# Kernel tuning notes

Measured on AMD Instinct MI355X. Metric: run time of the kernel, lower is better.

## Reference

```python
import jax, jax.numpy as jnp
import numpy as np

EPS = 1e-5
L = 8      # n_layers
H = 1024   # n_hidden
F_IN = 26  # input features
B = 65536  # batch


def layer_norm(x, gamma, beta):
    m = jnp.mean(x, axis=-1, keepdims=True)
    v = jnp.mean((x - m) ** 2, axis=-1, keepdims=True)
    return (x - m) * jax.lax.rsqrt(v + EPS) * gamma + beta


def setup_inputs() -> dict:
    key = jax.random.key(0)
    ks = jax.random.split(key, 12)
    s_in = 1.0 / np.sqrt(F_IN)
    s_h = 1.0 / np.sqrt(H)
    return {
        "x": jax.random.normal(ks[0], (B, F_IN), jnp.float32),
        "st_gamma": jnp.ones((F_IN,), jnp.float32),
        "st_beta": jnp.zeros((F_IN,), jnp.float32),
        "st_w": jax.random.uniform(ks[1], (H, F_IN), jnp.float32, -s_in, s_in),
        "st_b": jax.random.uniform(ks[2], (H,), jnp.float32, -s_in, s_in),
        "blk_gamma": jnp.ones((L, H), jnp.float32),
        "blk_beta": jnp.zeros((L, H), jnp.float32),
        "blk_w": jax.random.uniform(ks[3], (L, H, H), jnp.float32, -s_h, s_h),
        "blk_b": jax.random.uniform(ks[4], (L, H), jnp.float32, -s_h, s_h),
        "last_gamma": jnp.ones((H,), jnp.float32),
        "last_beta": jnp.zeros((H,), jnp.float32),
        "last_w": jax.random.uniform(ks[5], (1, H), jnp.float32, -s_h, s_h),
        "last_b": jax.random.uniform(ks[6], (1,), jnp.float32, -s_h, s_h),
    }


def reference(x, st_gamma, st_beta, st_w, st_b,
              blk_gamma, blk_beta, blk_w, blk_b,
              last_gamma, last_beta, last_w, last_b):
    # Stem: LN(26) -> Linear(26->H) -> ReLU (dropout = identity in eval)
    h = jax.nn.relu(layer_norm(x, st_gamma, st_beta) @ st_w.T + st_b)

    # n_layers blocks: LN -> Linear(H->H) -> ReLU, scanned over stacked params
    def body(h, params):
        g, b, w, bb = params
        h = jax.nn.relu(layer_norm(h, g, b) @ w.T + bb)
        return h, None

    h, _ = jax.lax.scan(body, h, (blk_gamma, blk_beta, blk_w, blk_b))

    # Head: LN -> Linear(H->1) -> sigmoid
    h = layer_norm(h, last_gamma, last_beta)
    out = jax.nn.sigmoid(h @ last_w.T + last_b)  # [B, 1]
    return out
```

## Files before the change

kernel.cpp:

```cpp
#include <hip/hip_runtime.h>
#include <hip/hip_bf16.h>
#include <stdint.h>


typedef __attribute__((ext_vector_type(8))) _Float16 f16x8;
typedef __attribute__((ext_vector_type(4))) float f32x4;

#define EPSLN 1e-5f
#define HDIM 1024

__device__ __forceinline__ void gload16(const void* g, void* l) {
  __builtin_amdgcn_global_load_lds(
      (const __attribute__((address_space(1))) unsigned int*)g,
      (__attribute__((address_space(3))) unsigned int*)l, 16, 0, 0);
}

__global__ __launch_bounds__(256) void zero_f32(float* __restrict__ p, int n) {
  int i = blockIdx.x * 256 + threadIdx.x;
  if (i < n) p[i] = 0.f;
}

__global__ __launch_bounds__(256) void fold_blk(
    const float* __restrict__ bg, const float* __restrict__ bb,
    const float* __restrict__ bw, const float* __restrict__ bbias,
    float* __restrict__ bfold, float* __restrict__ Sfold) {
  int lo = blockIdx.x;
  int layer = lo >> 10;
  const float* wrow = bw + (size_t)lo * HDIM;
  const float* g = bg + (size_t)layer * HDIM;
  const float* be = bb + (size_t)layer * HDIM;
  int t = threadIdx.x;
  float s = 0.f, acb = 0.f;
  for (int i = t; i < HDIM; i += 256) {
    float wv = wrow[i];
    _Float16 wp = (_Float16)(wv * g[i]);
    s += (float)wp;
    acb += be[i] * wv;
  }
#pragma unroll
  for (int off = 1; off < 64; off <<= 1) { s += __shfl_xor(s, off); acb += __shfl_xor(acb, off); }
  __shared__ float rs[4], rb[4];
  int l = t & 63, w = t >> 6;
  if (l == 0) { rs[w] = s; rb[w] = acb; }
  __syncthreads();
  if (t == 0) {
    Sfold[lo] = rs[0] + rs[1] + rs[2] + rs[3];
    bfold[lo] = bbias[lo] + rb[0] + rb[1] + rb[2] + rb[3];
  }
}

__global__ __launch_bounds__(256) void fold_pack(
    const float* __restrict__ bg, const float* __restrict__ bw,
    _Float16* __restrict__ Wfrag) {
  size_t tid = (size_t)blockIdx.x * 256 + threadIdx.x;
  int lay = (int)(tid >> 17);
  int oct = (int)(tid & 131071);
  int frag = oct >> 6, lane = oct & 63;
  int n16 = frag >> 5, kc = frag & 31;
  int o = n16 * 16 + (lane & 15);
  int ibase = kc * 32 + ((lane >> 4) << 3);
  const float* wrow = bw + ((size_t)lay << 20) + (size_t)o * HDIM + ibase;
  const float* g = bg + (size_t)lay * HDIM + ibase;
  f16x8 v;
#pragma unroll
  for (int j = 0; j < 8; ++j) v[j] = (_Float16)(wrow[j] * g[j]);
  *(f16x8*)(Wfrag + tid * 8) = v;
}

__global__ __launch_bounds__(256) void fold_head(
    const float* __restrict__ lg, const float* __restrict__ lb,
    const float* __restrict__ lw, const float* __restrict__ lbias,
    float* __restrict__ headW, float* __restrict__ headAux) {
  int t = threadIdx.x;
  float s = 0.f, acb = 0.f;
  for (int i = t; i < HDIM; i += 256) {
    float wp = lw[i] * lg[i];
    headW[i] = wp;
    s += wp;
    acb += lb[i] * lw[i];
  }
#pragma unroll
  for (int off = 1; off < 64; off <<= 1) { s += __shfl_xor(s, off); acb += __shfl_xor(acb, off); }
  __shared__ float rs[4], rb[4];
  int l = t & 63, w = t >> 6;
  if (l == 0) { rs[w] = s; rb[w] = acb; }
  __syncthreads();
  if (t == 0) {
    headAux[0] = rs[0] + rs[1] + rs[2] + rs[3];
    headAux[1] = lbias[0] + rb[0] + rb[1] + rb[2] + rb[3];
  }
}

__global__ __launch_bounds__(256) void fold_stem(const float* __restrict__ stw,
                                                 _Float16* __restrict__ Wst) {
  int idx = blockIdx.x * 256 + threadIdx.x;
  int o = idx >> 6, j = idx & 63;
  int i = (((j >> 3) ^ (o & 7)) << 3) + (j & 7);
  Wst[idx] = (i < 26) ? (_Float16)stw[o * 26 + i] : (_Float16)0.f;
}

__global__ __launch_bounds__(256) void stem_gemm(
    const float* __restrict__ x, const float* __restrict__ stg, const float* __restrict__ stb,
    const _Float16* __restrict__ Wst, const float* __restrict__ stbias,
    _Float16* __restrict__ hout, float* __restrict__ stats_out, int rowBase) {
  __shared__ float xin[128 * 26];
  __shared__ _Float16 As[128 * 64];
  __shared__ _Float16 Bs[128 * 64];
  const int t = threadIdx.x;
  const int l = t & 63;
  const int w = t >> 6;
  const int wm = w >> 1, wn = w & 1;
  const int brow = blockIdx.x * 128;
  const int bcol = blockIdx.y * 128;

  const _Float16* gb = Wst + (size_t)(bcol + (t >> 3)) * 64 + (t & 7) * 8;
  char* lB = (char*)Bs + (size_t)w * 1024;
#pragma unroll
  for (int q = 0; q < 4; ++q) gload16(gb + (size_t)q * 32 * 64, lB + q * 4096);

  const float* src = x + ((size_t)rowBase + brow) * 26;
  for (int i = t; i < 128 * 26; i += 256) xin[i] = src[i];
  __syncthreads();

  if (t < 128) {
    float m = 0.f;
#pragma unroll
    for (int i = 0; i < 26; ++i) m += xin[t * 26 + i];
    m *= (1.f / 26.f);
    float v = 0.f;
#pragma unroll
    for (int i = 0; i < 26; ++i) { float d = xin[t * 26 + i] - m; v += d * d; }
    float rstd = rsqrtf(v * (1.f / 26.f) + EPSLN);
    _Float16 tmp[32];
#pragma unroll
    for (int i = 0; i < 26; ++i)
      tmp[i] = (_Float16)((xin[t * 26 + i] - m) * rstd * stg[i] + stb[i]);
#pragma unroll
    for (int i = 26; i < 32; ++i) tmp[i] = (_Float16)0.f;
    char* arow = (char*)As + t * 128;
#pragma unroll
    for (int c = 0; c < 4; ++c) {
      f16x8 vv;
#pragma unroll
      for (int j = 0; j < 8; ++j) vv[j] = tmp[c * 8 + j];
      *(f16x8*)(arow + ((c ^ (t & 7)) << 4)) = vv;
    }
    f16x8 vz = (f16x8)(_Float16)0.f;
#pragma unroll
    for (int c = 4; c < 8; ++c) *(f16x8*)(arow + ((c ^ (t & 7)) << 4)) = vz;
  }
  __syncthreads();

  f32x4 acc[4][4];
#pragma unroll
  for (int i = 0; i < 4; ++i)
#pragma unroll
    for (int j = 0; j < 4; ++j) acc[i][j] = (f32x4){0.f, 0.f, 0.f, 0.f};

#pragma unroll
  for (int ks = 0; ks < 2; ++ks) {
    const int cx = ((ks * 4 + (l >> 4)) ^ (l & 7)) << 4;
    f16x8 af[4], bfr[4];
#pragma unroll
    for (int m = 0; m < 4; ++m)
      af[m] = *(const f16x8*)((const char*)As + (wm * 64 + m * 16 + (l & 15)) * 128 + cx);
#pragma unroll
    for (int n = 0; n < 4; ++n)
      bfr[n] = *(const f16x8*)((const char*)Bs + (wn * 64 + n * 16 + (l & 15)) * 128 + cx);
#pragma unroll
    for (int m = 0; m < 4; ++m)
#pragma unroll
      for (int n = 0; n < 4; ++n)
        acc[m][n] = __builtin_amdgcn_mfma_f32_16x16x32_f16(af[m], bfr[n], acc[m][n], 0, 0, 0);
  }

  __syncthreads();
  float* sred = (float*)xin;
  if (t < 256) sred[t] = 0.f;
  __syncthreads();

  float Bf[4];
#pragma unroll
  for (int n = 0; n < 4; ++n) Bf[n] = stbias[bcol + wn * 64 + n * 16 + (l & 15)];
#pragma unroll
  for (int m = 0; m < 4; ++m) {
#pragma unroll
    for (int rg = 0; rg < 4; ++rg) {
      int rloc = wm * 64 + m * 16 + (l >> 4) * 4 + rg;
      int lrow = brow + rloc;
      float ps = 0.f, psq = 0.f;
#pragma unroll
      for (int n = 0; n < 4; ++n) {
        int col = bcol + wn * 64 + n * 16 + (l & 15);
        float vv = fmaxf(acc[m][n][rg] + Bf[n], 0.f);
        hout[(size_t)lrow * HDIM + col] = (_Float16)vv;
        ps += vv; psq += vv * vv;
      }
#pragma unroll
      for (int off = 1; off < 16; off <<= 1) {
        ps += __shfl_xor(ps, off);
        psq += __shfl_xor(psq, off);
      }
      if ((l & 15) == 0) {
        atomicAdd(&sred[rloc * 2 + 0], ps);
        atomicAdd(&sred[rloc * 2 + 1], psq);
      }
    }
  }
  __syncthreads();
  if (t < 256) atomicAdd(&stats_out[(size_t)(brow + (t >> 1)) * 2 + (t & 1)], sred[t]);
}

__global__ __launch_bounds__(256, 4) void layer_gemm(
    const _Float16* __restrict__ hin, const float* __restrict__ stats_in,
    const _Float16* __restrict__ Wfrag, const float* __restrict__ bfold,
    const float* __restrict__ Sfold, _Float16* __restrict__ hout,
    float* __restrict__ stats_out) {
  __shared__ __align__(128) char smem[2 * 8192];
  const int t = threadIdx.x;
  const int l = t & 63;
  const int w = t >> 6;
  const int wm = w >> 1, wn = w & 1;
  int bid = blockIdx.x;
  {
    int nb = gridDim.x;
    if ((nb & 7) == 0) { int cpx = nb >> 3; bid = (bid & 7) * cpx + (bid >> 3); }
  }
  const int brow = (bid >> 3) * 128;
  const int bcol = (bid & 7) * 128;

  f32x4 acc[4][4];
#pragma unroll
  for (int i = 0; i < 4; ++i)
#pragma unroll
    for (int j = 0; j < 4; ++j) acc[i][j] = (f32x4){0.f, 0.f, 0.f, 0.f};

  const int cswz = (t & 3) ^ ((t >> 3) & 3);
  const _Float16* gA = hin + (size_t)(brow + (t >> 2)) * HDIM + cswz * 8;
  const int dstw = w << 10;

  auto stageA = [&](int kt) {
    char* dA = smem + (kt & 1) * 8192 + dstw;
    const _Float16* sA = gA + kt * 32;
    gload16(sA, dA);
    gload16(sA + (size_t)64 * HDIM, dA + 4096);
  };

  const _Float16* gBf = Wfrag + ((size_t)((bcol >> 4) + wn * 4) * 2048 + l) * 8;

  const int rl = l & 15;
  const int cx = (((l >> 4) ^ ((rl >> 1) & 3)) << 4);
  const int arow0 = wm * 4096 + rl * 64 + cx;

  f16x8 af[4], bf[4];

#define LOADB(kt)                                                              \
  do {                                                                         \
    _Pragma("unroll") for (int n = 0; n < 4; ++n)                              \
        bf[n] = *(const f16x8*)(gBf + (size_t)n * 16384 + (kt) * 512);         \
  } while (0)
#define DS_AF(kt)                                                              \
  do {                                                                         \
    const char* bc = smem + ((kt) & 1) * 8192;                                 \
    _Pragma("unroll") for (int m = 0; m < 4; ++m)                              \
        af[m] = *(const f16x8*)(bc + arow0 + m * 1024);                        \
  } while (0)
#define MFMA16()                                                               \
  do {                                                                         \
    __builtin_amdgcn_s_setprio(1);                                             \
    _Pragma("unroll") for (int m = 0; m < 4; ++m)                              \
        _Pragma("unroll") for (int n = 0; n < 4; ++n)                          \
            acc[m][n] = __builtin_amdgcn_mfma_f32_16x16x32_f16(af[m], bf[n],   \
                                                               acc[m][n], 0, 0, 0); \
    __builtin_amdgcn_s_setprio(0);                                             \
  } while (0)

  stageA(0);
  asm volatile("s_waitcnt vmcnt(0)" ::: "memory");
  __builtin_amdgcn_s_barrier();
  __builtin_amdgcn_sched_barrier(0);

#pragma unroll 1
  for (int kt = 0; kt < 31; ++kt) {
    LOADB(kt);
    stageA(kt + 1);
    DS_AF(kt);
    asm volatile("s_waitcnt vmcnt(2) lgkmcnt(0)" ::: "memory");
    __builtin_amdgcn_sched_barrier(0);
    MFMA16();
    __builtin_amdgcn_sched_barrier(0);
    asm volatile("s_waitcnt vmcnt(0)" ::: "memory");
    __builtin_amdgcn_s_barrier();
    __builtin_amdgcn_sched_barrier(0);
  }
  LOADB(31);
  DS_AF(31);
  asm volatile("s_waitcnt vmcnt(0) lgkmcnt(0)" ::: "memory");
  __builtin_amdgcn_sched_barrier(0);
  MFMA16();
  __syncthreads();

#undef LOADB
#undef DS_AF
#undef MFMA16

  float* sred = (float*)smem;
  sred[t] = 0.f;
  __syncthreads();

  float Sf[4], Bf2[4];
#pragma unroll
  for (int n = 0; n < 4; ++n) {
    int col = bcol + wn * 64 + n * 16 + rl;
    Sf[n] = Sfold[col];
    Bf2[n] = bfold[col];
  }
#pragma unroll
  for (int m = 0; m < 4; ++m) {
#pragma unroll
    for (int rg = 0; rg < 4; ++rg) {
      int rloc = wm * 64 + m * 16 + (l >> 4) * 4 + rg;
      int grow = brow + rloc;
      float sum = stats_in[(size_t)grow * 2 + 0];
      float sumsq = stats_in[(size_t)grow * 2 + 1];
      float mean = sum * (1.f / 1024.f);
      float rstd = rsqrtf(sumsq * (1.f / 1024.f) - mean * mean + EPSLN);
      float ps = 0.f, psq = 0.f;
#pragma unroll
      for (int n = 0; n < 4; ++n) {
        int col = bcol + wn * 64 + n * 16 + rl;
        float vv = rstd * (acc[m][n][rg] - mean * Sf[n]) + Bf2[n];
        vv = fmaxf(vv, 0.f);
        hout[(size_t)grow * HDIM + col] = (_Float16)vv;
        ps += vv; psq += vv * vv;
      }
#pragma unroll
      for (int off2 = 1; off2 < 16; off2 <<= 1) {
        ps += __shfl_xor(ps, off2);
        psq += __shfl_xor(psq, off2);
      }
      if (rl == 0) {
        atomicAdd(&sred[rloc * 2 + 0], ps);
        atomicAdd(&sred[rloc * 2 + 1], psq);
      }
    }
  }
  __syncthreads();
  atomicAdd(&stats_out[(size_t)(brow + (t >> 1)) * 2 + (t & 1)], sred[t]);
}

__global__ __launch_bounds__(512) void head_kernel(
    const _Float16* __restrict__ h8, const float* __restrict__ stats8,
    const float* __restrict__ headW, const float* __restrict__ headAux,
    float* __restrict__ out, int rowBase) {
  int t = threadIdx.x, l = t & 63, w = t >> 6;
  int lrow = blockIdx.x * 8 + w;
  const f16x8* hp = (const f16x8*)(h8 + (size_t)lrow * HDIM) + l * 2;
  f16x8 v0 = hp[0], v1 = hp[1];
  float acc = 0.f;
#pragma unroll
  for (int j = 0; j < 8; ++j) acc += (float)v0[j] * headW[l * 16 + j];
#pragma unroll
  for (int j = 0; j < 8; ++j) acc += (float)v1[j] * headW[l * 16 + 8 + j];
#pragma unroll
  for (int off = 1; off < 64; off <<= 1) acc += __shfl_xor(acc, off);
  if (l == 0) {
    float sum = stats8[lrow * 2 + 0], sumsq = stats8[lrow * 2 + 1];
    float mean = sum * (1.f / 1024.f);
    float rstd = rsqrtf(sumsq * (1.f / 1024.f) - mean * mean + EPSLN);
    float z = rstd * (acc - mean * headAux[0]) + headAux[1];
    out[rowBase + lrow] = 1.f / (1.f + expf(-z));
  }
}

extern "C" void kernel_launch(void* const* d_in, const int* in_sizes, int n_in,
                              void* d_out, int out_size, void* d_ws, size_t ws_size,
                              hipStream_t stream) {
  const float* x      = (const float*)d_in[0];
  const float* stg    = (const float*)d_in[1];
  const float* stb    = (const float*)d_in[2];
  const float* stw    = (const float*)d_in[3];
  const float* stbias = (const float*)d_in[4];
  const float* bg     = (const float*)d_in[5];
  const float* bb     = (const float*)d_in[6];
  const float* bw     = (const float*)d_in[7];
  const float* bbias  = (const float*)d_in[8];
  const float* lg     = (const float*)d_in[9];
  const float* lb     = (const float*)d_in[10];
  const float* lw     = (const float*)d_in[11];
  const float* lbias  = (const float*)d_in[12];
  float* out = (float*)d_out;
  const int B = 65536;
  const int L = 8;

  char* ws = (char*)d_ws;
  size_t off = 0;
  auto carve = [&](size_t bytes) -> char* {
    char* p = ws + off;
    off = (off + bytes + 255) & ~(size_t)255;
    return p;
  };
  _Float16* Wfrag = (_Float16*)carve((size_t)L * HDIM * HDIM * 2);
  float* bfold   = (float*)carve((size_t)L * HDIM * 4);
  float* Sfold   = (float*)carve((size_t)L * HDIM * 4);
  float* headW   = (float*)carve((size_t)HDIM * 4);
  float* headAux = (float*)carve(256);
  _Float16* Wst  = (_Float16*)carve((size_t)HDIM * 64 * 2);
  size_t fixed = off;

  int R = B;
  while (R > 256) {
    size_t need = fixed + 2 * ((size_t)R * HDIM * 2 + 256) + ((size_t)9 * R * 2 * 4 + 256);
    if (need <= ws_size) break;
    R >>= 1;
  }
  _Float16* hA = (_Float16*)carve((size_t)R * HDIM * 2);
  _Float16* hB = (_Float16*)carve((size_t)R * HDIM * 2);
  float* stats = (float*)carve((size_t)9 * R * 2 * 4);

  fold_blk<<<L * HDIM, 256, 0, stream>>>(bg, bb, bw, bbias, bfold, Sfold);
  fold_pack<<<(L * 131072) / 256, 256, 0, stream>>>(bg, bw, Wfrag);
  fold_head<<<1, 256, 0, stream>>>(lg, lb, lw, lbias, headW, headAux);
  fold_stem<<<HDIM * 64 / 256, 256, 0, stream>>>(stw, Wst);

  const int nstats = 9 * R * 2;
  for (int c = 0; c < B / R; ++c) {
    int rowBase = c * R;
    zero_f32<<<(nstats + 255) / 256, 256, 0, stream>>>(stats, nstats);
    {
      dim3 grid(R / 128, 8);
      stem_gemm<<<grid, 256, 0, stream>>>(x, stg, stb, Wst, stbias, hA, stats, rowBase);
    }
    _Float16* cur = hA;
    _Float16* nxt = hB;
    for (int lyr = 0; lyr < L; ++lyr) {
      int nb = (R / 128) * 8;
      layer_gemm<<<nb, 256, 0, stream>>>(
          cur, stats + (size_t)lyr * R * 2, Wfrag + (size_t)lyr * HDIM * HDIM,
          bfold + lyr * HDIM, Sfold + lyr * HDIM, nxt, stats + (size_t)(lyr + 1) * R * 2);
      _Float16* tmp = cur; cur = nxt; nxt = tmp;
    }
    head_kernel<<<R / 8, 512, 0, stream>>>(cur, stats + (size_t)8 * R * 2, headW, headAux, out, rowBase);
  }
}
```

Before: 1.469 ms.

## Store activations in MFMA 32x32 fragment layout and load operands directly from global

Measured after the change: 1.751 ms. +19.2%, slower.

```diff
diff --git a/kernel.cpp b/kernel.cpp
--- a/kernel.cpp
+++ b/kernel.cpp
@@ -5,6 +5,7 @@
 
 typedef __attribute__((ext_vector_type(8))) _Float16 f16x8;
 typedef __attribute__((ext_vector_type(4))) float f32x4;
+typedef __attribute__((ext_vector_type(16))) float f32x16;
 
 #define EPSLN 1e-5f
 #define HDIM 1024
@@ -49,22 +50,22 @@
   }
 }
 
-__global__ __launch_bounds__(256) void fold_pack(
+__global__ __launch_bounds__(256) void fold_pack32(
     const float* __restrict__ bg, const float* __restrict__ bw,
-    _Float16* __restrict__ Wfrag) {
+    _Float16* __restrict__ Wf) {
   size_t tid = (size_t)blockIdx.x * 256 + threadIdx.x;
   int lay = (int)(tid >> 17);
   int oct = (int)(tid & 131071);
   int frag = oct >> 6, lane = oct & 63;
-  int n16 = frag >> 5, kc = frag & 31;
-  int o = n16 * 16 + (lane & 15);
-  int ibase = kc * 32 + ((lane >> 4) << 3);
-  const float* wrow = bw + ((size_t)lay << 20) + (size_t)o * HDIM + ibase;
-  const float* g = bg + (size_t)lay * HDIM + ibase;
+  int n32 = frag >> 6, kc = frag & 63;
+  int col = n32 * 32 + (lane & 31);
+  int kbase = kc * 16 + ((lane >> 5) << 3);
+  const float* wrow = bw + ((size_t)lay << 20) + (size_t)col * HDIM + kbase;
+  const float* g = bg + (size_t)lay * HDIM + kbase;
   f16x8 v;
 #pragma unroll
   for (int j = 0; j < 8; ++j) v[j] = (_Float16)(wrow[j] * g[j]);
-  *(f16x8*)(Wfrag + tid * 8) = v;
+  *(f16x8*)(Wf + tid * 8) = v;
 }
 
 __global__ __launch_bounds__(256) void fold_head(
@@ -102,7 +103,7 @@
 __global__ __launch_bounds__(256) void stem_gemm(
     const float* __restrict__ x, const float* __restrict__ stg, const float* __restrict__ stb,
     const _Float16* __restrict__ Wst, const float* __restrict__ stbias,
-    _Float16* __restrict__ hout, float* __restrict__ stats_out, int rowBase) {
+    _Float16* __restrict__ hP, float* __restrict__ stats_out, int rowBase) {
   __shared__ float xin[128 * 26];
   __shared__ _Float16 As[128 * 64];
   __shared__ _Float16 Bs[128 * 64];
@@ -187,13 +188,15 @@
 #pragma unroll
     for (int rg = 0; rg < 4; ++rg) {
       int rloc = wm * 64 + m * 16 + (l >> 4) * 4 + rg;
-      int lrow = brow + rloc;
+      int rbW = (brow >> 5) + (rloc >> 5);
       float ps = 0.f, psq = 0.f;
 #pragma unroll
       for (int n = 0; n < 4; ++n) {
         int col = bcol + wn * 64 + n * 16 + (l & 15);
         float vv = fmaxf(acc[m][n][rg] + Bf[n], 0.f);
-        hout[(size_t)lrow * HDIM + col] = (_Float16)vv;
+        size_t flat = (((size_t)rbW * 64 + (col >> 4)) * 64 +
+                       ((rloc & 31) + 32 * ((l >> 3) & 1))) * 8 + (l & 7);
+        hP[flat] = (_Float16)vv;
         ps += vv; psq += vv * vv;
       }
 #pragma unroll
@@ -211,12 +214,13 @@
   if (t < 256) atomicAdd(&stats_out[(size_t)(brow + (t >> 1)) * 2 + (t & 1)], sred[t]);
 }
 
-__global__ __launch_bounds__(256, 4) void layer_gemm(
-    const _Float16* __restrict__ hin, const float* __restrict__ stats_in,
-    const _Float16* __restrict__ Wfrag, const float* __restrict__ bfold,
-    const float* __restrict__ Sfold, _Float16* __restrict__ hout,
+__global__ __launch_bounds__(256) void layer32(
+    const _Float16* __restrict__ hPin, const float* __restrict__ stats_in,
+    const _Float16* __restrict__ Wf, const float* __restrict__ bfold,
+    const float* __restrict__ Sfold, _Float16* __restrict__ hPout,
     float* __restrict__ stats_out) {
-  __shared__ __align__(128) char smem[2 * 8192];
+  __shared__ float mrstd[256];
+  __shared__ float sred[256];
   const int t = threadIdx.x;
   const int l = t & 63;
   const int w = t >> 6;
@@ -229,119 +233,114 @@
   const int brow = (bid >> 3) * 128;
   const int bcol = (bid & 7) * 128;
 
-  f32x4 acc[4][4];
-#pragma unroll
-  for (int i = 0; i < 4; ++i)
-#pragma unroll
-    for (int j = 0; j < 4; ++j) acc[i][j] = (f32x4){0.f, 0.f, 0.f, 0.f};
-
-  const int cswz = (t & 3) ^ ((t >> 3) & 3);
-  const _Float16* gA = hin + (size_t)(brow + (t >> 2)) * HDIM + cswz * 8;
-  const int dstw = w << 10;
-
-  auto stageA = [&](int kt) {
-    char* dA = smem + (kt & 1) * 8192 + dstw;
-    const _Float16* sA = gA + kt * 32;
-    gload16(sA, dA);
-    gload16(sA + (size_t)64 * HDIM, dA + 4096);
-  };
-
-  const _Float16* gBf = Wfrag + ((size_t)((bcol >> 4) + wn * 4) * 2048 + l) * 8;
-
-  const int rl = l & 15;
-  const int cx = (((l >> 4) ^ ((rl >> 1) & 3)) << 4);
-  const int arow0 = wm * 4096 + rl * 64 + cx;
-
-  f16x8 af[4], bf[4];
-
-#define LOADB(kt)                                                              \
-  do {                                                                         \
-    _Pragma("unroll") for (int n = 0; n < 4; ++n)                              \
-        bf[n] = *(const f16x8*)(gBf + (size_t)n * 16384 + (kt) * 512);         \
+  if (t < 128) {
+    float sum = stats_in[(size_t)(brow + t) * 2 + 0];
+    float sumsq = stats_in[(size_t)(brow + t) * 2 + 1];
+    float mean = sum * (1.f / 1024.f);
+    mrstd[t * 2 + 0] = mean;
+    mrstd[t * 2 + 1] = rsqrtf(sumsq * (1.f / 1024.f) - mean * mean + EPSLN);
+  }
+  sred[t] = 0.f;
+  __syncthreads();
+
+  f32x16 acc[2][2];
+#pragma unroll
+  for (int i = 0; i < 2; ++i)
+#pragma unroll
+    for (int j = 0; j < 2; ++j)
+#pragma unroll
+      for (int e = 0; e < 16; ++e) acc[i][j][e] = 0.f;
+
+  const int rb0 = (brow >> 5) + wm * 2;
+  const int n0 = (bcol >> 5) + wn * 2;
+  const _Float16* Abase = hPin + ((size_t)rb0 * 4096 + l) * 8;
+  const _Float16* Bbase = Wf + ((size_t)n0 * 4096 + l) * 8;
+
+  f16x8 A0[2][2], B0[2][2], A1[2][2], B1[2][2];
+
+#define LOADT(A_, B_, kt)                                                        \
+  do {                                                                           \
+    const int kc2 = (kt) * 2;                                                    \
+    _Pragma("unroll") for (int pm = 0; pm < 2; ++pm)                             \
+        _Pragma("unroll") for (int h = 0; h < 2; ++h)                            \
+            A_[pm][h] = *(const f16x8*)(Abase + pm * 32768 + (kc2 + h) * 512);   \
+    _Pragma("unroll") for (int pn = 0; pn < 2; ++pn)                             \
+        _Pragma("unroll") for (int h = 0; h < 2; ++h)                            \
+            B_[pn][h] = *(const f16x8*)(Bbase + pn * 32768 + (kc2 + h) * 512);   \
   } while (0)
-#define DS_AF(kt)                                                              \
-  do {                                                                         \
-    const char* bc = smem + ((kt) & 1) * 8192;                                 \
-    _Pragma("unroll") for (int m = 0; m < 4; ++m)                              \
-        af[m] = *(const f16x8*)(bc + arow0 + m * 1024);                        \
+#define COMPUTE(A_, B_)                                                          \
+  do {                                                                           \
+    __builtin_amdgcn_s_setprio(1);                                               \
+    _Pragma("unroll") for (int pm = 0; pm < 2; ++pm)                             \
+        _Pragma("unroll") for (int pn = 0; pn < 2; ++pn) {                       \
+      acc[pm][pn] = __builtin_amdgcn_mfma_f32_32x32x16_f16(A_[pm][0], B_[pn][0], \
+                                                           acc[pm][pn], 0, 0, 0);\
+      acc[pm][pn] = __builtin_amdgcn_mfma_f32_32x32x16_f16(A_[pm][1], B_[pn][1], \
+                                                           acc[pm][pn], 0, 0, 0);\
+    }                                                                            \
+    __builtin_amdgcn_s_setprio(0);                                               \
   } while (0)
-#define MFMA16()                                                               \
-  do {                                                                         \
-    __builtin_amdgcn_s_setprio(1);                                             \
-    _Pragma("unroll") for (int m = 0; m < 4; ++m)                              \
-        _Pragma("unroll") for (int n = 0; n < 4; ++n)                          \
-            acc[m][n] = __builtin_amdgcn_mfma_f32_16x16x32_f16(af[m], bf[n],   \
-                                                               acc[m][n], 0, 0, 0); \
-    __builtin_amdgcn_s_setprio(0);                                             \
+#define WAITN(N)                                                \
+  do {                                                          \
+    asm volatile("s_waitcnt vmcnt(" #N ")" ::: "memory");       \
+    __builtin_amdgcn_sched_barrier(0);                          \
   } while (0)
 
-  stageA(0);
-  asm volatile("s_waitcnt vmcnt(0)" ::: "memory");
-  __builtin_amdgcn_s_barrier();
-  __builtin_amdgcn_sched_barrier(0);
-
+  LOADT(A0, B0, 0);
 #pragma unroll 1
-  for (int kt = 0; kt < 31; ++kt) {
-    LOADB(kt);
-    stageA(kt + 1);
-    DS_AF(kt);
-    asm volatile("s_waitcnt vmcnt(2) lgkmcnt(0)" ::: "memory");
-    __builtin_amdgcn_sched_barrier(0);
-    MFMA16();
-    __builtin_amdgcn_sched_barrier(0);
-    asm volatile("s_waitcnt vmcnt(0)" ::: "memory");
-    __builtin_amdgcn_s_barrier();
-    __builtin_amdgcn_sched_barrier(0);
-  }
-  LOADB(31);
-  DS_AF(31);
-  asm volatile("s_waitcnt vmcnt(0) lgkmcnt(0)" ::: "memory");
-  __builtin_amdgcn_sched_barrier(0);
-  MFMA16();
-  __syncthreads();
-
-#undef LOADB
-#undef DS_AF
-#undef MFMA16
-
-  float* sred = (float*)smem;
-  sred[t] = 0.f;
-  __syncthreads();
-
-  float Sf[4], Bf2[4];
-#pragma unroll
-  for (int n = 0; n < 4; ++n) {
-    int col = bcol + wn * 64 + n * 16 + rl;
-    Sf[n] = Sfold[col];
-    Bf2[n] = bfold[col];
-  }
-#pragma unroll
-  for (int m = 0; m < 4; ++m) {
-#pragma unroll
-    for (int rg = 0; rg < 4; ++rg) {
-      int rloc = wm * 64 + m * 16 + (l >> 4) * 4 + rg;
-      int grow = brow + rloc;
-      float sum = stats_in[(size_t)grow * 2 + 0];
-      float sumsq = stats_in[(size_t)grow * 2 + 1];
-      float mean = sum * (1.f / 1024.f);
-      float rstd = rsqrtf(sumsq * (1.f / 1024.f) - mean * mean + EPSLN);
-      float ps = 0.f, psq = 0.f;
-#pragma unroll
-      for (int n = 0; n < 4; ++n) {
-        int col = bcol + wn * 64 + n * 16 + rl;
-        float vv = rstd * (acc[m][n][rg] - mean * Sf[n]) + Bf2[n];
+  for (int kt2 = 0; kt2 < 15; ++kt2) {
+    LOADT(A1, B1, 2 * kt2 + 1);
+    WAITN(8);
+    COMPUTE(A0, B0);
+    LOADT(A0, B0, 2 * kt2 + 2);
+    WAITN(8);
+    COMPUTE(A1, B1);
+  }
+  LOADT(A1, B1, 31);
+  WAITN(8);
+  COMPUTE(A0, B0);
+  WAITN(0);
+  COMPUTE(A1, B1);
+
+#undef LOADT
+#undef COMPUTE
+#undef WAITN
+
+  float Sc[2], Bc[2];
+#pragma unroll
+  for (int pn = 0; pn < 2; ++pn) {
+    int col = bcol + wn * 64 + pn * 32 + (l & 31);
+    Sc[pn] = Sfold[col];
+    Bc[pn] = bfold[col];
+  }
+  const int hw = (l >> 3) & 1, jj = l & 7;
+#pragma unroll
+  for (int pm = 0; pm < 2; ++pm) {
+    const int rbW = (brow >> 5) + wm * 2 + pm;
+#pragma unroll
+    for (int reg = 0; reg < 16; ++reg) {
+      int rr = (reg & 3) + 8 * (reg >> 2) + 4 * (l >> 5);
+      int rloc = wm * 64 + pm * 32 + rr;
+      float mean = mrstd[rloc * 2 + 0];
+      float rstd = mrstd[rloc * 2 + 1];
+      float s = 0.f, sq = 0.f;
+#pragma unroll
+      for (int pn = 0; pn < 2; ++pn) {
+        float vv = rstd * (acc[pm][pn][reg] - mean * Sc[pn]) + Bc[pn];
         vv = fmaxf(vv, 0.f);
-        hout[(size_t)grow * HDIM + col] = (_Float16)vv;
-        ps += vv; psq += vv * vv;
-      }
-#pragma unroll
-      for (int off2 = 1; off2 < 16; off2 <<= 1) {
-        ps += __shfl_xor(ps, off2);
-        psq += __shfl_xor(psq, off2);
-      }
-      if (rl == 0) {
-        atomicAdd(&sred[rloc * 2 + 0], ps);
-        atomicAdd(&sred[rloc * 2 + 1], psq);
+        int kc = (bcol >> 4) + wn * 4 + pn * 2 + ((l >> 4) & 1);
+        size_t flat = (((size_t)rbW * 64 + kc) * 64 + (rr + 32 * hw)) * 8 + jj;
+        hPout[flat] = (_Float16)vv;
+        s += vv; sq += vv * vv;
+      }
+#pragma unroll
+      for (int off = 1; off < 32; off <<= 1) {
+        s += __shfl_xor(s, off);
+        sq += __shfl_xor(sq, off);
+      }
+      if ((l & 31) == 0) {
+        atomicAdd(&sred[rloc * 2 + 0], s);
+        atomicAdd(&sred[rloc * 2 + 1], sq);
       }
     }
   }
@@ -350,13 +349,14 @@
 }
 
 __global__ __launch_bounds__(512) void head_kernel(
-    const _Float16* __restrict__ h8, const float* __restrict__ stats8,
+    const _Float16* __restrict__ h8P, const float* __restrict__ stats8,
     const float* __restrict__ headW, const float* __restrict__ headAux,
     float* __restrict__ out, int rowBase) {
   int t = threadIdx.x, l = t & 63, w = t >> 6;
   int lrow = blockIdx.x * 8 + w;
-  const f16x8* hp = (const f16x8*)(h8 + (size_t)lrow * HDIM) + l * 2;
-  f16x8 v0 = hp[0], v1 = hp[1];
+  const _Float16* hp = h8P + (((size_t)(lrow >> 5) * 64 + l) * 64 + (lrow & 31)) * 8;
+  f16x8 v0 = *(const f16x8*)hp;
+  f16x8 v1 = *(const f16x8*)(hp + 256);
   float acc = 0.f;
 #pragma unroll
   for (int j = 0; j < 8; ++j) acc += (float)v0[j] * headW[l * 16 + j];
@@ -400,7 +400,7 @@
     off = (off + bytes + 255) & ~(size_t)255;
     return p;
   };
-  _Float16* Wfrag = (_Float16*)carve((size_t)L * HDIM * HDIM * 2);
+  _Float16* Wf32  = (_Float16*)carve((size_t)L * HDIM * HDIM * 2);
   float* bfold   = (float*)carve((size_t)L * HDIM * 4);
   float* Sfold   = (float*)carve((size_t)L * HDIM * 4);
   float* headW   = (float*)carve((size_t)HDIM * 4);
@@ -419,7 +419,7 @@
   float* stats = (float*)carve((size_t)9 * R * 2 * 4);
 
   fold_blk<<<L * HDIM, 256, 0, stream>>>(bg, bb, bw, bbias, bfold, Sfold);
-  fold_pack<<<(L * 131072) / 256, 256, 0, stream>>>(bg, bw, Wfrag);
+  fold_pack32<<<(L * 131072) / 256, 256, 0, stream>>>(bg, bw, Wf32);
   fold_head<<<1, 256, 0, stream>>>(lg, lb, lw, lbias, headW, headAux);
   fold_stem<<<HDIM * 64 / 256, 256, 0, stream>>>(stw, Wst);
 
@@ -435,8 +435,8 @@
     _Float16* nxt = hB;
     for (int lyr = 0; lyr < L; ++lyr) {
       int nb = (R / 128) * 8;
-      layer_gemm<<<nb, 256, 0, stream>>>(
-          cur, stats + (size_t)lyr * R * 2, Wfrag + (size_t)lyr * HDIM * HDIM,
+      layer32<<<nb, 256, 0, stream>>>(
+          cur, stats + (size_t)lyr * R * 2, Wf32 + (size_t)lyr * HDIM * HDIM,
           bfold + lyr * HDIM, Sfold + lyr * HDIM, nxt, stats + (size_t)(lyr + 1) * R * 2);
       _Float16* tmp = cur; cur = nxt; nxt = tmp;
     }
```
